# Kernel optimization log

Hardware: AMD Instinct MI355X
Metric: run time of the kernel (lower is better)

Reference implementation:

```python
import jax, jax.numpy as jnp
import numpy as np

CHANNELS = 1024
PIVOT = 16384


def setup_inputs() -> dict:
    key = jax.random.key(0)
    k1, k2, k3 = jax.random.split(key, 3)
    x_Jx = jax.random.normal(k1, (3 * PIVOT, CHANNELS), dtype=jnp.float32)
    # Linear(channels, channels) params, torch-like init scale
    s = 1.0 / np.sqrt(CHANNELS)
    W = jax.random.uniform(k2, (CHANNELS, CHANNELS), dtype=jnp.float32, minval=-s, maxval=s)
    b = jax.random.uniform(k3, (CHANNELS,), dtype=jnp.float32, minval=-s, maxval=s)
    return {"x_Jx": x_Jx, "W": W, "b": b}


def reference(x_Jx, W, b):
    pivot = x_Jx.shape[0] // 3
    channels = W.shape[0]
    x = x_Jx[:pivot]                                   # [P, C]
    hAx = jnp.tanh(x @ W.T + b)                        # [P, C]
    hpAx = 1.0 - hAx ** 2                              # tanh'
    Jx = x_Jx[pivot:].reshape(pivot, channels, 2)      # [P, C, 2]
    # sum_j W[i,j] * Jx[p,j,k]  (the explicit broadcast-sum in torch is this GEMM)
    WJx = jnp.einsum('ij,pjk->pik', W, Jx)             # [P, C, 2]
    hpAJx = (hpAx[:, :, None] * WJx).reshape(-1, channels)  # [2P, C]
    return jnp.concatenate([hAx, hpAJx], axis=0)       # [3P, C]
```

## Files before the change

kernel.cpp:

```cpp
#include <hip/hip_runtime.h>
#include <hip/hip_bf16.h>
#include <cstdint>

typedef __attribute__((ext_vector_type(8))) short short8;
typedef __attribute__((ext_vector_type(4))) float floatx4;

__device__ __forceinline__ float tanh_fast(float x) {
    float e = __expf(2.0f * x);
    return 1.0f - 2.0f * __builtin_amdgcn_rcpf(e + 1.0f);
}

__device__ __forceinline__ unsigned int bf16_bits(float f) {
    __hip_bfloat16 h = __float2bfloat16(f);
    return (unsigned int)*reinterpret_cast<unsigned short*>(&h);
}
__device__ __forceinline__ unsigned int pack2(float lo, float hi) {
    return bf16_bits(lo) | (bf16_bits(hi) << 16);
}

__device__ __forceinline__ void async16(const void* g, void* l) {
    __builtin_amdgcn_global_load_lds(
        (const __attribute__((address_space(1))) unsigned int*)g,
        (__attribute__((address_space(3))) unsigned int*)l, 16, 0, 0);
}

__device__ __forceinline__ void swizzle_tile_bm(int& row0, int& col0, int bm) {
    const int gx   = gridDim.x;
    const int nwg  = gx * gridDim.y;
    const int flat = blockIdx.y * gx + blockIdx.x;
    const int swz  = (flat & 7) * (nwg >> 3) + (flat >> 3);
    col0 = (swz % gx) * bm;
    row0 = (swz / gx) * bm;
}


__global__ __launch_bounds__(256) void cvt_prep(
    const float* __restrict__ X, const float* __restrict__ G,
    const float* __restrict__ W,
    short* __restrict__ Xb, short* __restrict__ Mb, short* __restrict__ Wb,
    int nbX, int nbG)
{
    const int tid = threadIdx.x;
    const int b   = blockIdx.x;
    if (b < nbX) {
        const size_t e = ((size_t)b * 256 + tid) * 16;
        const float4 f0 = *(const float4*)(X + e);
        const float4 f1 = *(const float4*)(X + e + 4);
        const float4 f2 = *(const float4*)(X + e + 8);
        const float4 f3 = *(const float4*)(X + e + 12);
        uint4 o0, o1;
        o0.x = pack2(f0.x, f0.y); o0.y = pack2(f0.z, f0.w);
        o0.z = pack2(f1.x, f1.y); o0.w = pack2(f1.z, f1.w);
        o1.x = pack2(f2.x, f2.y); o1.y = pack2(f2.z, f2.w);
        o1.z = pack2(f3.x, f3.y); o1.w = pack2(f3.z, f3.w);
        *(uint4*)(Xb + e)     = o0;
        *(uint4*)(Xb + e + 8) = o1;
    } else if (b < nbX + nbG) {
        const size_t s = (size_t)(b - nbX) * 256 + tid;
        const size_t p = s >> 7;
        const int    c = (int)(s & 127);
        const float* src = G + p * 2048 + (size_t)c * 16;
        const float4 f0 = *(const float4*)(src);
        const float4 f1 = *(const float4*)(src + 4);
        const float4 f2 = *(const float4*)(src + 8);
        const float4 f3 = *(const float4*)(src + 12);
        uint4 E, O;
        E.x = pack2(f0.x, f0.z); E.y = pack2(f1.x, f1.z);
        E.z = pack2(f2.x, f2.z); E.w = pack2(f3.x, f3.z);
        O.x = pack2(f0.y, f0.w); O.y = pack2(f1.y, f1.w);
        O.z = pack2(f2.y, f2.w); O.w = pack2(f3.y, f3.w);
        *(uint4*)(Mb + (2 * p)     * 1024 + (size_t)c * 8) = E;
        *(uint4*)(Mb + (2 * p + 1) * 1024 + (size_t)c * 8) = O;
    } else {
        const size_t e = ((size_t)(b - nbX - nbG) * 256 + tid) * 16;
        const float4 f0 = *(const float4*)(W + e);
        const float4 f1 = *(const float4*)(W + e + 4);
        const float4 f2 = *(const float4*)(W + e + 8);
        const float4 f3 = *(const float4*)(W + e + 12);
        uint4 o0, o1;
        o0.x = pack2(f0.x, f0.y); o0.y = pack2(f0.z, f0.w);
        o0.z = pack2(f1.x, f1.y); o0.w = pack2(f1.z, f1.w);
        o1.x = pack2(f2.x, f2.y); o1.y = pack2(f2.z, f2.w);
        o1.z = pack2(f3.x, f3.y); o1.w = pack2(f3.z, f3.w);
        *(uint4*)(Wb + e)     = o0;
        *(uint4*)(Wb + e + 8) = o1;
    }
}

#define STAGE256(dst_d, kt)                                                    \
    {                                                                          \
        const int koff = (kt) * 64;                                            \
        _Pragma("unroll")                                                      \
        for (int i = 0; i < 4; ++i) {                                          \
            async16(Ag + (size_t)(i * 64) * K + koff,                          \
                    As + (dst_d) * 16384 + (i * 64 + wave * 8) * 64);          \
            async16(Bg + (size_t)(i * 64) * K + koff,                          \
                    Bs + (dst_d) * 16384 + (i * 64 + wave * 8) * 64);          \
        }                                                                      \
    }

#define GEMM256_MAIN()                                                         \
    {                                                                          \
        const int NT = K >> 6;                                                 \
        STAGE256(0, 0)                                                         \
        asm volatile("s_waitcnt vmcnt(0)" ::: "memory");                       \
        __builtin_amdgcn_s_barrier();                                          \
        for (int t = 0; t < NT; ++t) {                                         \
            const int d = t & 1;                                               \
            if (t + 1 < NT) STAGE256(d ^ 1, t + 1)                             \
            const short* Ad = As + d * 16384;                                  \
            const short* Bd = Bs + d * 16384;                                  \
            short8 bfr[4][2];                                                  \
            _Pragma("unroll")                                                  \
            for (int n = 0; n < 4; ++n)                                        \
                _Pragma("unroll")                                              \
                for (int ki = 0; ki < 2; ++ki)                                 \
                    bfr[n][ki] = *(const short8*)&Bd[b_base + n * 1024 +       \
                                     (((ki * 4 + quad) ^ rxor) * 8)];          \
            _Pragma("unroll")                                                  \
            for (int p = 0; p < 4; ++p) {                                      \
                short8 afr[2][2];                                              \
                _Pragma("unroll")                                              \
                for (int a2 = 0; a2 < 2; ++a2)                                 \
                    _Pragma("unroll")                                          \
                    for (int ki = 0; ki < 2; ++ki)                             \
                        afr[a2][ki] = *(const short8*)&Ad[a_base +             \
                            (p * 2 + a2) * 1024 +                              \
                            (((ki * 4 + quad) ^ rxor) * 8)];                   \
                __builtin_amdgcn_s_setprio(1);                                 \
                _Pragma("unroll")                                              \
                for (int a2 = 0; a2 < 2; ++a2)                                 \
                    _Pragma("unroll")                                          \
                    for (int n = 0; n < 4; ++n)                                \
                        _Pragma("unroll")                                      \
                        for (int ki = 0; ki < 2; ++ki)                         \
                            acc[p * 2 + a2][n] =                               \
                                __builtin_amdgcn_mfma_f32_16x16x32_bf16(       \
                                    afr[a2][ki], bfr[n][ki],                   \
                                    acc[p * 2 + a2][n], 0, 0, 0);              \
                __builtin_amdgcn_s_setprio(0);                                 \
            }                                                                  \
            asm volatile("s_waitcnt vmcnt(0)" ::: "memory");                   \
            __builtin_amdgcn_s_barrier();                                      \
        }                                                                      \
    }

__global__ __launch_bounds__(512, 1) void k1c_gemm_tanh(
    const short* __restrict__ A,
    const short* __restrict__ B,
    const float* __restrict__ Bv,
    float* __restrict__ out, int K)
{
    __shared__ __align__(16) short As[2 * 256 * 64];
    __shared__ __align__(16) short Bs[2 * 256 * 64];

    const int tid  = threadIdx.x;
    const int lane = tid & 63;
    const int wave = tid >> 6;
    const int wr = wave >> 2, wc = wave & 3;

    int row0, col0;
    swizzle_tile_bm(row0, col0, 256);

    const int l15  = lane & 15;
    const int quad = lane >> 4;
    const int rxor = l15 & 7;
    const int a_base = (wr * 128 + l15) * 64;
    const int b_base = (wc * 64  + l15) * 64;

    const int lrow = lane >> 3;
    const int lcol = lane & 7;
    const int cswz = lcol ^ lrow;
    const short* Ag = A + (size_t)(row0 + wave * 8 + lrow) * K + cswz * 8;
    const short* Bg = B + (size_t)(col0 + wave * 8 + lrow) * K + cswz * 8;

    floatx4 acc[8][4];
#pragma unroll
    for (int a = 0; a < 8; ++a)
#pragma unroll
        for (int n = 0; n < 4; ++n) acc[a][n] = (floatx4){0.f, 0.f, 0.f, 0.f};

    GEMM256_MAIN()

    float bv[4];
#pragma unroll
    for (int n = 0; n < 4; ++n)
        bv[n] = Bv[col0 + wc * 64 + n * 16 + l15];

#pragma unroll
    for (int a = 0; a < 8; ++a) {
        const int rbase = row0 + wr * 128 + a * 16 + quad * 4;
#pragma unroll
        for (int n = 0; n < 4; ++n) {
            const int c = col0 + wc * 64 + n * 16 + l15;
#pragma unroll
            for (int r = 0; r < 4; ++r)
                out[(size_t)(rbase + r) * 1024 + c] = tanh_fast(acc[a][n][r] + bv[n]);
        }
    }
}

__global__ __launch_bounds__(512, 1) void k2c_gemm_jac(
    const short* __restrict__ A,
    const short* __restrict__ B,
    const float* __restrict__ Hout,
    float* __restrict__ out2, int K)
{
    __shared__ __align__(16) short As[2 * 256 * 64];
    __shared__ __align__(16) short Bs[2 * 256 * 64];

    const int tid  = threadIdx.x;
    const int lane = tid & 63;
    const int wave = tid >> 6;
    const int wr = wave >> 2, wc = wave & 3;

    int r0, col0;
    swizzle_tile_bm(r0, col0, 256);

    const int l15  = lane & 15;
    const int quad = lane >> 4;
    const int rxor = l15 & 7;
    const int a_base = (wr * 128 + l15) * 64;
    const int b_base = (wc * 64  + l15) * 64;

    const int lrow = lane >> 3;
    const int lcol = lane & 7;
    const int cswz = lcol ^ lrow;
    const short* Ag = A + (size_t)(r0 + wave * 8 + lrow) * K + cswz * 8;
    const short* Bg = B + (size_t)(col0 + wave * 8 + lrow) * K + cswz * 8;

    floatx4 acc[8][4];
#pragma unroll
    for (int a = 0; a < 8; ++a)
#pragma unroll
        for (int n = 0; n < 4; ++n) acc[a][n] = (floatx4){0.f, 0.f, 0.f, 0.f};

    GEMM256_MAIN()

#pragma unroll
    for (int a = 0; a < 8; ++a) {
        const int rb = r0 + wr * 128 + a * 16 + quad * 4;
#pragma unroll
        for (int n = 0; n < 4; ++n) {
            const int i = col0 + wc * 64 + n * 16 + l15;
            const int shift = (i >= 512) ? 1 : 0;
            const int ccol = 2 * i - shift * 1024;
#pragma unroll
            for (int pr = 0; pr < 2; ++pr) {
                const int re = rb + pr * 2;
                const int p  = re >> 1;
                const float h  = Hout[(size_t)p * 1024 + i];
                const float hp = 1.0f - h * h;
                float2 st;
                st.x = hp * acc[a][n][pr * 2];
                st.y = hp * acc[a][n][pr * 2 + 1];
                *(float2*)&out2[(size_t)(re + shift) * 1024 + ccol] = st;
            }
        }
    }
}

#define LDS_STRIDE 72

__device__ __forceinline__ void swizzle_tile(int& row0, int& col0) {
    const int nwg  = gridDim.x * gridDim.y;
    const int flat = blockIdx.y * gridDim.x + blockIdx.x;
    const int swz  = (flat & 7) * (nwg >> 3) + (flat >> 3);
    col0 = (swz & 7) * 128;
    row0 = (swz >> 3) * 128;
}

__global__ __launch_bounds__(256) void k1_gemm_tanh(
    const float* __restrict__ X, const float* __restrict__ W,
    const float* __restrict__ Bv, float* __restrict__ out, int K)
{
    __shared__ __align__(16) short As[128 * LDS_STRIDE];
    __shared__ __align__(16) short Bs[128 * LDS_STRIDE];
    const int tid  = threadIdx.x;
    const int lane = tid & 63;
    const int wave = tid >> 6;
    const int wm = wave & 1, wn = wave >> 1;
    int row0, col0;
    swizzle_tile(row0, col0);
    const int l15  = lane & 15;
    const int quad = lane >> 4;
    const int a_base = (wm * 64 + l15) * LDS_STRIDE;
    const int b_base = (wn * 64 + l15) * LDS_STRIDE;

    floatx4 acc[4][4];
#pragma unroll
    for (int a = 0; a < 4; ++a)
#pragma unroll
        for (int b = 0; b < 4; ++b) acc[a][b] = (floatx4){0.f, 0.f, 0.f, 0.f};

    for (int k0 = 0; k0 < K; k0 += 64) {
        __syncthreads();
#pragma unroll
        for (int i = 0; i < 8; ++i) {
            const int g = i * 256 + tid;
            const int r = g >> 4, c = g & 15;
            const float4 va = *(const float4*)(X + (size_t)(row0 + r) * K + k0 + c * 4);
            const float4 vb = *(const float4*)(W + (size_t)(col0 + r) * K + k0 + c * 4);
            uint2 ea, eb;
            ea.x = pack2(va.x, va.y); ea.y = pack2(va.z, va.w);
            eb.x = pack2(vb.x, vb.y); eb.y = pack2(vb.z, vb.w);
            *(uint2*)&As[r * LDS_STRIDE + c * 4] = ea;
            *(uint2*)&Bs[r * LDS_STRIDE + c * 4] = eb;
        }
        __syncthreads();
#pragma unroll
        for (int ki = 0; ki < 2; ++ki) {
            const int kx = ki * 32 + quad * 8;
            short8 af[4], bf[4];
#pragma unroll
            for (int s = 0; s < 4; ++s)
                af[s] = *(const short8*)&As[a_base + s * 16 * LDS_STRIDE + kx];
#pragma unroll
            for (int s = 0; s < 4; ++s)
                bf[s] = *(const short8*)&Bs[b_base + s * 16 * LDS_STRIDE + kx];
#pragma unroll
            for (int a = 0; a < 4; ++a)
#pragma unroll
                for (int b = 0; b < 4; ++b)
                    acc[a][b] = __builtin_amdgcn_mfma_f32_16x16x32_bf16(
                        af[a], bf[b], acc[a][b], 0, 0, 0);
        }
    }

    float bv[4];
#pragma unroll
    for (int b = 0; b < 4; ++b)
        bv[b] = Bv[col0 + wn * 64 + b * 16 + l15];
#pragma unroll
    for (int a = 0; a < 4; ++a) {
        const int rbase = row0 + wm * 64 + a * 16 + quad * 4;
#pragma unroll
        for (int b = 0; b < 4; ++b) {
            const int n = col0 + wn * 64 + b * 16 + l15;
#pragma unroll
            for (int r = 0; r < 4; ++r)
                out[(size_t)(rbase + r) * 1024 + n] = tanh_fast(acc[a][b][r] + bv[b]);
        }
    }
}

__global__ __launch_bounds__(256) void k2_gemm_jac(
    const float* __restrict__ G, const float* __restrict__ W,
    const float* __restrict__ Hout, float* __restrict__ out2, int K)
{
    __shared__ __align__(16) short As[128 * LDS_STRIDE];
    __shared__ __align__(16) short Bs[128 * LDS_STRIDE];
    const int tid  = threadIdx.x;
    const int lane = tid & 63;
    const int wave = tid >> 6;
    const int wm = wave & 1, wn = wave >> 1;
    int r0, col0;
    swizzle_tile(r0, col0);
    const int p0 = r0 >> 1;
    const int l15  = lane & 15;
    const int quad = lane >> 4;
    const int a_base = (wm * 64 + l15) * LDS_STRIDE;
    const int b_base = (wn * 64 + l15) * LDS_STRIDE;

    floatx4 acc[4][4];
#pragma unroll
    for (int a = 0; a < 4; ++a)
#pragma unroll
        for (int b = 0; b < 4; ++b) acc[a][b] = (floatx4){0.f, 0.f, 0.f, 0.f};

    for (int k0 = 0; k0 < K; k0 += 64) {
        __syncthreads();
#pragma unroll
        for (int i = 0; i < 8; ++i) {
            const int g = i * 256 + tid;
            const int r = g >> 4, c = g & 15;
            const float4 vb = *(const float4*)(W + (size_t)(col0 + r) * K + k0 + c * 4);
            uint2 eb;
            eb.x = pack2(vb.x, vb.y); eb.y = pack2(vb.z, vb.w);
            *(uint2*)&Bs[r * LDS_STRIDE + c * 4] = eb;
        }
#pragma unroll
        for (int i = 0; i < 4; ++i) {
            const int g = i * 256 + tid;
            const int q = g >> 4, d = g & 15;
            const float* src = G + (size_t)(p0 + q) * 2048 + 2 * k0 + d * 8;
            const float4 u0 = *(const float4*)src;
            const float4 u1 = *(const float4*)(src + 4);
            uint2 E, O;
            E.x = pack2(u0.x, u0.z); E.y = pack2(u1.x, u1.z);
            O.x = pack2(u0.y, u0.w); O.y = pack2(u1.y, u1.w);
            *(uint2*)&As[(2 * q)     * LDS_STRIDE + d * 4] = E;
            *(uint2*)&As[(2 * q + 1) * LDS_STRIDE + d * 4] = O;
        }
        __syncthreads();
#pragma unroll
        for (int ki = 0; ki < 2; ++ki) {
            const int kx = ki * 32 + quad * 8;
            short8 af[4], bf[4];
#pragma unroll
            for (int s = 0; s < 4; ++s)
                af[s] = *(const short8*)&As[a_base + s * 16 * LDS_STRIDE + kx];
#pragma unroll
            for (int s = 0; s < 4; ++s)
                bf[s] = *(const short8*)&Bs[b_base + s * 16 * LDS_STRIDE + kx];
#pragma unroll
            for (int a = 0; a < 4; ++a)
#pragma unroll
                for (int b = 0; b < 4; ++b)
                    acc[a][b] = __builtin_amdgcn_mfma_f32_16x16x32_bf16(
                        af[a], bf[b], acc[a][b], 0, 0, 0);
        }
    }

#pragma unroll
    for (int a = 0; a < 4; ++a) {
        const int rb = r0 + wm * 64 + a * 16 + quad * 4;
#pragma unroll
        for (int b = 0; b < 4; ++b) {
            const int i = col0 + wn * 64 + b * 16 + l15;
            const int shift = (i >= 512) ? 1 : 0;
            const int ccol = 2 * i - shift * 1024;
#pragma unroll
            for (int pr = 0; pr < 2; ++pr) {
                const int re = rb + pr * 2;
                const int p  = re >> 1;
                const float h  = Hout[(size_t)p * 1024 + i];
                const float hp = 1.0f - h * h;
                float2 st;
                st.x = hp * acc[a][b][pr * 2];
                st.y = hp * acc[a][b][pr * 2 + 1];
                *(float2*)&out2[(size_t)(re + shift) * 1024 + ccol] = st;
            }
        }
    }
}

extern "C" void kernel_launch(void* const* d_in, const int* in_sizes, int n_in,
                              void* d_out, int out_size, void* d_ws, size_t ws_size,
                              hipStream_t stream) {
    const float* xJx = (const float*)d_in[0];
    const float* W   = (const float*)d_in[1];
    const float* bv  = (const float*)d_in[2];
    float* out = (float*)d_out;

    const int C     = 1024;
    const int rows3 = in_sizes[0] / C;
    const int pivot = rows3 / 3;

    const size_t szXb = (size_t)pivot * C * 2;
    const size_t szMb = (size_t)2 * pivot * C * 2;
    const size_t szWb = (size_t)C * C * 2;

    if (ws_size >= szXb + szMb + szWb) {
        short* Xb = (short*)d_ws;
        short* Mb = (short*)((char*)d_ws + szXb);
        short* Wb = (short*)((char*)d_ws + szXb + szMb);

        const int nbX = (pivot * C) / 4096;
        const int nbG = (pivot * 2 * C) / 4096;
        const int nbW = (C * C) / 4096;
        cvt_prep<<<dim3(nbX + nbG + nbW), dim3(256), 0, stream>>>(
            xJx, xJx + (size_t)pivot * C, W, Xb, Mb, Wb, nbX, nbG);

        dim3 g1(C / 256, pivot / 256);
        k1c_gemm_tanh<<<g1, dim3(512), 0, stream>>>(Xb, Wb, bv, out, C);

        dim3 g2(C / 256, (2 * pivot) / 256);
        k2c_gemm_jac<<<g2, dim3(512), 0, stream>>>(Mb, Wb, out,
                                                   out + (size_t)pivot * C, C);
    } else {
        dim3 g1(C / 128, pivot / 128);
        k1_gemm_tanh<<<g1, dim3(256), 0, stream>>>(xJx, W, bv, out, C);
        dim3 g2(C / 128, (2 * pivot) / 128);
        k2_gemm_jac<<<g2, dim3(256), 0, stream>>>(xJx + (size_t)pivot * C, W, out,
                                                  out + (size_t)pivot * C, C);
    }
}
```

Measured before the change: 483.9 us.

## Split GEMM main loop into barrier-separated phases interleaving loads with MFMA

Restructures the double-buffered GEMM inner loop into phases. The next-tile A prefetch is issued after the B fragment reads in phase 0, and the B prefetch in phase 1. Workgroup barriers are added around each MFMA cluster so waves run in lockstep, alternating LDS reads and matrix math in the style of an 8-phase ping-pong schedule. The aim is to spread global-to-LDS traffic and reduce contention between LDS reads and MFMA issue. The cost is several extra barriers per K tile, which may add stalls with one workgroup per CU.

```diff
diff --git a/kernel.cpp b/kernel.cpp
--- a/kernel.cpp
+++ b/kernel.cpp
@@ -87,38 +87,45 @@
     }
 }
 
-#define STAGE256(dst_d, kt)                                                    \
+#define STAGE_A256(dst_d, kt)                                                  \
     {                                                                          \
-        const int koff = (kt) * 64;                                            \
         _Pragma("unroll")                                                      \
-        for (int i = 0; i < 4; ++i) {                                          \
-            async16(Ag + (size_t)(i * 64) * K + koff,                          \
+        for (int i = 0; i < 4; ++i)                                            \
+            async16(Ag + (size_t)(i * 64) * K + (kt) * 64,                     \
                     As + (dst_d) * 16384 + (i * 64 + wave * 8) * 64);          \
-            async16(Bg + (size_t)(i * 64) * K + koff,                          \
+    }
+#define STAGE_B256(dst_d, kt)                                                  \
+    {                                                                          \
+        _Pragma("unroll")                                                      \
+        for (int i = 0; i < 4; ++i)                                            \
+            async16(Bg + (size_t)(i * 64) * K + (kt) * 64,                     \
                     Bs + (dst_d) * 16384 + (i * 64 + wave * 8) * 64);          \
-        }                                                                      \
-    }
-
-#define GEMM256_MAIN()                                                         \
+    }
+
+#define GEMM256_8PH()                                                          \
     {                                                                          \
         const int NT = K >> 6;                                                 \
-        STAGE256(0, 0)                                                         \
+        STAGE_A256(0, 0) STAGE_B256(0, 0)                                      \
         asm volatile("s_waitcnt vmcnt(0)" ::: "memory");                       \
         __builtin_amdgcn_s_barrier();                                          \
         for (int t = 0; t < NT; ++t) {                                         \
             const int d = t & 1;                                               \
-            if (t + 1 < NT) STAGE256(d ^ 1, t + 1)                             \
             const short* Ad = As + d * 16384;                                  \
             const short* Bd = Bs + d * 16384;                                  \
             short8 bfr[4][2];                                                  \
             _Pragma("unroll")                                                  \
-            for (int n = 0; n < 4; ++n)                                        \
-                _Pragma("unroll")                                              \
-                for (int ki = 0; ki < 2; ++ki)                                 \
-                    bfr[n][ki] = *(const short8*)&Bd[b_base + n * 1024 +       \
-                                     (((ki * 4 + quad) ^ rxor) * 8)];          \
-            _Pragma("unroll")                                                  \
             for (int p = 0; p < 4; ++p) {                                      \
+                if (p == 0) {                                                  \
+                    _Pragma("unroll")                                          \
+                    for (int n = 0; n < 4; ++n)                                \
+                        _Pragma("unroll")                                      \
+                        for (int ki = 0; ki < 2; ++ki)                         \
+                            bfr[n][ki] = *(const short8*)&Bd[b_base +          \
+                                n * 1024 + (((ki * 4 + quad) ^ rxor) * 8)];    \
+                    if (t + 1 < NT) STAGE_A256(d ^ 1, t + 1)                   \
+                } else if (p == 1) {                                           \
+                    if (t + 1 < NT) STAGE_B256(d ^ 1, t + 1)                   \
+                }                                                              \
                 short8 afr[2][2];                                              \
                 _Pragma("unroll")                                              \
                 for (int a2 = 0; a2 < 2; ++a2)                                 \
@@ -127,6 +134,7 @@
                         afr[a2][ki] = *(const short8*)&Ad[a_base +             \
                             (p * 2 + a2) * 1024 +                              \
                             (((ki * 4 + quad) ^ rxor) * 8)];                   \
+                __builtin_amdgcn_s_barrier();                                  \
                 __builtin_amdgcn_s_setprio(1);                                 \
                 _Pragma("unroll")                                              \
                 for (int a2 = 0; a2 < 2; ++a2)                                 \
@@ -139,6 +147,7 @@
                                     afr[a2][ki], bfr[n][ki],                   \
                                     acc[p * 2 + a2][n], 0, 0, 0);              \
                 __builtin_amdgcn_s_setprio(0);                                 \
+                if (p < 3) __builtin_amdgcn_s_barrier();                       \
             }                                                                  \
             asm volatile("s_waitcnt vmcnt(0)" ::: "memory");                   \
             __builtin_amdgcn_s_barrier();                                      \
@@ -180,7 +189,7 @@
 #pragma unroll
         for (int n = 0; n < 4; ++n) acc[a][n] = (floatx4){0.f, 0.f, 0.f, 0.f};
 
-    GEMM256_MAIN()
+    GEMM256_8PH()
 
     float bv[4];
 #pragma unroll
@@ -235,7 +244,7 @@
 #pragma unroll
         for (int n = 0; n < 4; ++n) acc[a][n] = (floatx4){0.f, 0.f, 0.f, 0.f};
 
-    GEMM256_MAIN()
+    GEMM256_8PH()
 
 #pragma unroll
     for (int a = 0; a < 8; ++a) {
```

Measured after the change: 476.5 us. Within noise of the previous version (-1.5%).
